# Performance work log

Hardware: AMD Instinct MI355X
Metric: run time of the kernel (lower is better)

Reference implementation:

```python
import jax, jax.numpy as jnp
import numpy as np

B, C, T, V = 64, 64, 128, 25   # batch, in_channels, frames, joints
R = 8                          # rel_channels = in_channels // rel_reduction
TS = 9                         # time_step (temporal taps of dynamic adjacency)
OUT = 64                       # out_channels (conv3)


def setup_inputs() -> dict:
    key = jax.random.key(0)
    ks = jax.random.split(key, 10)
    p = lambda k, shape: jax.random.normal(k, shape, jnp.float32) * 0.05
    return {
        'x':  jax.random.normal(ks[0], (B, C, T, V), jnp.float32),
        'A':  jax.random.normal(ks[1], (V, V), jnp.float32) * 0.1,
        'W1': p(ks[2], (R, C)),       'b1': p(ks[3], (R,)),
        'W2': p(ks[4], (R, C)),       'b2': p(ks[5], (R,)),
        'W4': p(ks[6], (C * TS, R)),  'b4': p(ks[7], (C * TS,)),
        'W3': p(ks[8], (OUT, C)),     'b3': p(ks[9], (OUT,)),
    }


def reference(x, A, W1, b1, W2, b2, W4, b4, W3, b3):
    alpha = 1.0
    # conv1/conv2: 1x1 Conv2d then mean over time (dim -2). 1x1 conv is linear,
    # so mean(conv(x)) == einsum/T + bias.  -> (B, R, V)
    x1 = jnp.einsum('rc,bctv->brv', W1, x) / T + b1[None, :, None]
    x2 = jnp.einsum('rc,bctv->brv', W2, x) / T + b2[None, :, None]
    # tanh relation: (B, R, V, 1) - (B, R, 1, V) -> (B, R, V, V)
    rel = jnp.tanh(x1[:, :, :, None] - x2[:, :, None, :])
    # conv4 (1x1): rel_channels -> C*TS dynamic adjacency, + static A
    Adyn = jnp.einsum('or,brij->boij', W4, rel) + b4[None, :, None, None]
    Adyn = Adyn * alpha + A[None, None]                      # (B, C*TS, V, V)
    # reshape(B, C, TS, V, V).permute(0,1,3,4,2): per-(b,c) temporal graph kernel
    Wk = Adyn.reshape(B, C, TS, V, V).transpose(0, 1, 3, 4, 2)  # (B, C, V, V, TS)
    # x -> (B, C, V, T), causal left-pad by TS-1 (matches F.pad(x, (TS-1, 0)))
    xp = jnp.pad(x.transpose(0, 1, 3, 2), ((0, 0), (0, 0), (0, 0), (TS - 1, 0)))
    # Grouped conv1d loop over V vertices, fused into TS tap-wise einsums:
    # z[b,c,t,i] = sum_{v,k} xp[b,c,v,t+k] * Wk[b,c,v,i,k]   (stride=1)
    z = jnp.zeros((B, C, T, V), x.dtype)
    for k in range(TS):  # small fixed tap loop
        z = z + jnp.einsum('bcvt,bcvi->bcti', xp[..., k:k + T], Wk[..., k])
    # conv3: 1x1 Conv2d C -> OUT
    out = jnp.einsum('oc,bctv->botv', W3, z) + b3[None, :, None, None]
    return out
```

## Files before the change

kernel.cpp:

```cpp
#include <hip/hip_runtime.h>
#include <hip/hip_bf16.h>

#define BB 64
#define CC 64
#define TT_ 128
#define VV 25
#define RR 8
#define TS_ 9
#define OO 64
#define VCH 5

typedef __hip_bfloat16 bf16;
typedef __attribute__((ext_vector_type(8))) short short8;
typedef __attribute__((ext_vector_type(4))) short s16x4;
typedef __attribute__((ext_vector_type(4))) float f32x4;

__device__ __forceinline__ unsigned short f2b(float f) {
    bf16 h = __float2bfloat16(f);
    return __builtin_bit_cast(unsigned short, h);
}

__global__ __launch_bounds__(256) void k_mean(const float* __restrict__ x,
                                              float* __restrict__ xm) {
    __shared__ float smf[800];
    int bc = blockIdx.x;
    int tid = threadIdx.x;
    const float4* p4 = (const float4*)(x + (size_t)bc * TT_ * VV);
    if (tid < 200) {
        float4 a = p4[tid];
        float4 b = p4[tid + 200];
        float4 c = p4[tid + 400];
        float4 d = p4[tid + 600];
        float4 s;
        s.x = a.x + b.x + c.x + d.x;
        s.y = a.y + b.y + c.y + d.y;
        s.z = a.z + b.z + c.z + d.z;
        s.w = a.w + b.w + c.w + d.w;
        ((float4*)smf)[tid] = s;
    }
    __syncthreads();
    if (tid < VV) {
        float tot = 0.f;
        #pragma unroll
        for (int m = 0; m < 32; m++) tot += smf[tid + VV * m];
        xm[bc * VV + tid] = tot * (1.0f / TT_);
    }
}

__global__ __launch_bounds__(256) void k_rel(const float* __restrict__ xm,
                                             const float* __restrict__ W1,
                                             const float* __restrict__ b1,
                                             const float* __restrict__ W2,
                                             const float* __restrict__ b2,
                                             float* __restrict__ rel) {
    __shared__ float xms[CC * VV];
    __shared__ float x1s[RR][VCH];
    __shared__ float x2s[RR][VV];
    int b = blockIdx.x / 5, g = blockIdx.x % 5;
    int v0 = g * VCH;
    int tid = threadIdx.x;
    for (int i = tid; i < CC * VV; i += 256) xms[i] = xm[b * CC * VV + i];
    __syncthreads();
    if (tid < 240) {
        if (tid < 40) {
            int r = tid / VCH, vl = tid % VCH;
            float s1 = b1[r];
            for (int c = 0; c < CC; c++) s1 += W1[r * CC + c] * xms[c * VV + v0 + vl];
            x1s[r][vl] = s1;
        } else {
            int t = tid - 40;
            int r = t / VV, i = t % VV;
            float s2 = b2[r];
            for (int c = 0; c < CC; c++) s2 += W2[r * CC + c] * xms[c * VV + i];
            x2s[r][i] = s2;
        }
    }
    __syncthreads();
    float* relb = rel + (size_t)b * VV * VV * RR + (size_t)v0 * VV * RR;
    for (int idx = tid; idx < VCH * VV * RR; idx += 256) {
        int r = idx % RR;
        int i = (idx / RR) % VV;
        int vl = idx / (RR * VV);
        float d = x1s[r][vl] - x2s[r][i];
        float e = __expf(2.0f * d);
        relb[idx] = (e - 1.0f) / (e + 1.0f);
    }
}

__global__ __launch_bounds__(512, 8) void k_z(const float* __restrict__ x,
                                              const float* __restrict__ Ag,
                                              const float* __restrict__ W4,
                                              const float* __restrict__ b4,
                                              const float* __restrict__ rel,
                                              bf16* __restrict__ zws) {
    __shared__ __align__(16) unsigned short xpadB[136 * 40];
    __shared__ __align__(16) unsigned short AdbS[TS_ * 32 * 40];

    int tid = threadIdx.x;
    int bc = blockIdx.x;
    int b = bc / CC, c = bc % CC;

    if (tid < 128) ((unsigned int*)xpadB)[(tid >> 4) * 20 + (tid & 15)] = 0u;
    if (tid >= 128 && tid < 256) {
        int base = (8 + (tid - 128)) * 40 + 25;
        #pragma unroll
        for (int k = 0; k < 7; k++) xpadB[base + k] = 0;
    }
    if (tid >= 224) {
        int base = (tid - 224) * 40 + 25;
        #pragma unroll
        for (int k = 0; k < 7; k++) AdbS[base + k] = 0;
    }
    const float4* xg4 = (const float4*)(x + (size_t)bc * TT_ * VV);
    for (int i4 = tid; i4 < TT_ * VV / 4; i4 += 512) {
        float4 f = xg4[i4];
        int idx = i4 * 4;
        int t = idx / VV, v = idx - t * VV;
        float fe[4] = {f.x, f.y, f.z, f.w};
        #pragma unroll
        for (int e = 0; e < 4; e++) {
            xpadB[(t + 8) * 40 + v] = f2b(fe[e]);
            v++;
            if (v == VV) { v = 0; t++; }
        }
    }

    const float* relb = rel + (size_t)b * VV * VV * RR;
    const float* W4c = W4 + c * TS_ * RR;
    const float* b4c = b4 + c * TS_;
    for (int task = tid; task < VV * VV; task += 512) {
        int v = task / VV, i = task % VV;
        const float4* r4 = (const float4*)(relb + (size_t)task * RR);
        float4 ra = r4[0], rb_ = r4[1];
        float av = Ag[task];
        #pragma unroll
        for (int s = 0; s < TS_; s++) {
            float a2 = b4c[s] + av;
            a2 += W4c[s*8+0] * ra.x  + W4c[s*8+1] * ra.y
                + W4c[s*8+2] * ra.z  + W4c[s*8+3] * ra.w;
            a2 += W4c[s*8+4] * rb_.x + W4c[s*8+5] * rb_.y
                + W4c[s*8+6] * rb_.z + W4c[s*8+7] * rb_.w;
            AdbS[(s * 32 + i) * 40 + v] = f2b(a2);
        }
    }
    __syncthreads();

    int lane = tid & 63, wv = tid >> 6;
    int ml = lane & 15, qd = lane >> 4;
    f32x4 acc00 = {0.f, 0.f, 0.f, 0.f};
    f32x4 acc01 = acc00;
    int rowA0 = wv * 16 + ml;
    #pragma unroll
    for (int s = 0; s < TS_; s++) {
        short8 a0 = *(const short8*)&xpadB[(rowA0 + s) * 40 + qd * 8];
        short8 b0 = *(const short8*)&AdbS[(s * 32 + ml) * 40 + qd * 8];
        short8 b1 = *(const short8*)&AdbS[(s * 32 + 16 + ml) * 40 + qd * 8];
        acc00 = __builtin_amdgcn_mfma_f32_16x16x32_bf16(a0, b0, acc00, 0, 0, 0);
        acc01 = __builtin_amdgcn_mfma_f32_16x16x32_bf16(a0, b1, acc01, 0, 0, 0);
    }

    bf16* zb = zws + (size_t)bc * TT_ * VV;
    int t0 = wv * 16 + qd * 4;
    int i0 = ml, i1 = 16 + ml;
    #pragma unroll
    for (int r = 0; r < 4; r++)
        zb[(t0 + r) * VV + i0] = __float2bfloat16(acc00[r]);
    if (i1 < VV) {
        #pragma unroll
        for (int r = 0; r < 4; r++)
            zb[(t0 + r) * VV + i1] = __float2bfloat16(acc01[r]);
    }
}

__global__ __launch_bounds__(256) void k_conv3(const bf16* __restrict__ zws,
                                               const float* __restrict__ W3,
                                               const float* __restrict__ b3,
                                               float* __restrict__ out) {
    __shared__ __align__(16) unsigned short w3b[OO * 72];
    __shared__ __align__(16) unsigned short zl[CC * 130];
    __shared__ float b3l[OO];
    int tid = threadIdx.x;
    int b = blockIdx.x / 25, tile = blockIdx.x % 25;
    int tj0 = tile * 128;

    if (tid < OO) b3l[tid] = b3[tid];
    const float4* W3v = (const float4*)W3;
    for (int idx = tid; idx < OO * CC / 4; idx += 256) {
        float4 f = W3v[idx];
        int o = idx >> 4, c4 = (idx & 15) * 4;
        s16x4 s4;
        s4[0] = (short)f2b(f.x);
        s4[1] = (short)f2b(f.y);
        s4[2] = (short)f2b(f.z);
        s4[3] = (short)f2b(f.w);
        *(s16x4*)&w3b[o * 72 + c4] = s4;
    }
    const unsigned int* zg = (const unsigned int*)(zws + (size_t)b * CC * (TT_ * VV));
    for (int idu = tid; idu < CC * 64; idu += 256) {
        int c = idu >> 6, ju = idu & 63;
        ((unsigned int*)zl)[c * 65 + ju] = zg[c * 1600 + (tj0 >> 1) + ju];
    }
    __syncthreads();

    int lane = tid & 63, wv = tid >> 6;
    int ml = lane & 15, qd = lane >> 4;
    f32x4 acc[4][2];
    #pragma unroll
    for (int m = 0; m < 4; m++)
        #pragma unroll
        for (int nl = 0; nl < 2; nl++) acc[m][nl] = (f32x4){0.f, 0.f, 0.f, 0.f};

    #pragma unroll
    for (int k0 = 0; k0 < 2; k0++) {
        short8 a[4];
        #pragma unroll
        for (int m = 0; m < 4; m++)
            a[m] = *(const short8*)&w3b[(m * 16 + ml) * 72 + k0 * 32 + qd * 8];
        #pragma unroll
        for (int nl = 0; nl < 2; nl++) {
            int col = (2 * wv + nl) * 16 + ml;
            int cb = k0 * 32 + qd * 8;
            short8 bf;
            #pragma unroll
            for (int j = 0; j < 8; j++)
                bf[j] = (short)zl[(cb + j) * 130 + col];
            #pragma unroll
            for (int m = 0; m < 4; m++)
                acc[m][nl] = __builtin_amdgcn_mfma_f32_16x16x32_bf16(a[m], bf, acc[m][nl], 0, 0, 0);
        }
    }

    float* ob = out + (size_t)b * OO * (TT_ * VV) + tj0;
    #pragma unroll
    for (int m = 0; m < 4; m++)
        #pragma unroll
        for (int nl = 0; nl < 2; nl++) {
            int col = (2 * wv + nl) * 16 + ml;
            #pragma unroll
            for (int r = 0; r < 4; r++) {
                int o = m * 16 + qd * 4 + r;
                ob[(size_t)o * (TT_ * VV) + col] = acc[m][nl][r] + b3l[o];
            }
        }
}

extern "C" void kernel_launch(void* const* d_in, const int* in_sizes, int n_in,
                              void* d_out, int out_size, void* d_ws, size_t ws_size,
                              hipStream_t stream) {
    const float* x  = (const float*)d_in[0];
    const float* A  = (const float*)d_in[1];
    const float* W1 = (const float*)d_in[2];
    const float* b1 = (const float*)d_in[3];
    const float* W2 = (const float*)d_in[4];
    const float* b2 = (const float*)d_in[5];
    const float* W4 = (const float*)d_in[6];
    const float* b4 = (const float*)d_in[7];
    const float* W3 = (const float*)d_in[8];
    const float* b3 = (const float*)d_in[9];
    float* out = (float*)d_out;

    char* ws = (char*)d_ws;
    float* xm   = (float*)(ws);
    float* rel  = (float*)(ws + 409600);
    bf16*  zws  = (bf16*)(ws + 1689600);

    k_mean <<<BB * CC, 256, 0, stream>>>(x, xm);
    k_rel  <<<BB * 5,  256, 0, stream>>>(xm, W1, b1, W2, b2, rel);
    k_z    <<<BB * CC, 512, 0, stream>>>(x, A, W4, b4, rel, zws);
    k_conv3<<<BB * 25, 256, 0, stream>>>(zws, W3, b3, out);
}
```

Measured before the change: 162.9 us.

## Pre-pack padded bf16 x in k_mean and DMA it into LDS in k_z

k_mean, which already reads x, now also converts it to bf16 in the padded LDS layout that k_z needs and writes that image to a workspace buffer. k_z then loads the ready-made tile straight into LDS with global_load_lds instead of re-reading fp32 x and converting element by element. This halves the bytes k_z reads for x and removes its scattered conversion stores. In exchange k_mean writes an extra bf16 copy of x, k_z's occupancy hint of 8 is dropped, and correctness relies on the global-to-LDS loads completing before the existing barrier.

```diff
diff --git a/kernel.cpp b/kernel.cpp
--- a/kernel.cpp
+++ b/kernel.cpp
@@ -9,6 +9,7 @@
 #define TS_ 9
 #define OO 64
 #define VCH 5
+#define XBF_STRIDE 5632
 
 typedef __hip_bfloat16 bf16;
 typedef __attribute__((ext_vector_type(8))) short short8;
@@ -20,23 +21,45 @@
     return __builtin_bit_cast(unsigned short, h);
 }
 
+__device__ __forceinline__ void putf4(unsigned short* xp, int i4, float4 f) {
+    int idx = i4 * 4;
+    int t = idx / VV, v = idx - t * VV;
+    float fe[4] = {f.x, f.y, f.z, f.w};
+    #pragma unroll
+    for (int e = 0; e < 4; e++) {
+        xp[(t + 8) * 40 + v] = f2b(fe[e]);
+        if (++v == VV) { v = 0; t++; }
+    }
+}
+
 __global__ __launch_bounds__(256) void k_mean(const float* __restrict__ x,
-                                              float* __restrict__ xm) {
+                                              float* __restrict__ xm,
+                                              unsigned short* __restrict__ xbf) {
     __shared__ float smf[800];
+    __shared__ __align__(16) unsigned short xp[141 * 40];
     int bc = blockIdx.x;
     int tid = threadIdx.x;
     const float4* p4 = (const float4*)(x + (size_t)bc * TT_ * VV);
+    float4 a, b, c, d;
     if (tid < 200) {
-        float4 a = p4[tid];
-        float4 b = p4[tid + 200];
-        float4 c = p4[tid + 400];
-        float4 d = p4[tid + 600];
+        a = p4[tid];
+        b = p4[tid + 200];
+        c = p4[tid + 400];
+        d = p4[tid + 600];
+    }
+    for (int i = tid; i < 2820; i += 256) ((unsigned int*)xp)[i] = 0u;
+    __syncthreads();
+    if (tid < 200) {
         float4 s;
         s.x = a.x + b.x + c.x + d.x;
         s.y = a.y + b.y + c.y + d.y;
         s.z = a.z + b.z + c.z + d.z;
         s.w = a.w + b.w + c.w + d.w;
         ((float4*)smf)[tid] = s;
+        putf4(xp, tid,       a);
+        putf4(xp, tid + 200, b);
+        putf4(xp, tid + 400, c);
+        putf4(xp, tid + 600, d);
     }
     __syncthreads();
     if (tid < VV) {
@@ -45,6 +68,9 @@
         for (int m = 0; m < 32; m++) tot += smf[tid + VV * m];
         xm[bc * VV + tid] = tot * (1.0f / TT_);
     }
+    uint4* dst = (uint4*)(xbf + (size_t)bc * XBF_STRIDE);
+    const uint4* src = (const uint4*)xp;
+    for (int i = tid; i < 704; i += 256) dst[i] = src[i];
 }
 
 __global__ __launch_bounds__(256) void k_rel(const float* __restrict__ xm,
@@ -87,42 +113,35 @@
     }
 }
 
-__global__ __launch_bounds__(512, 8) void k_z(const float* __restrict__ x,
-                                              const float* __restrict__ Ag,
-                                              const float* __restrict__ W4,
-                                              const float* __restrict__ b4,
-                                              const float* __restrict__ rel,
-                                              bf16* __restrict__ zws) {
-    __shared__ __align__(16) unsigned short xpadB[136 * 40];
+__global__ __launch_bounds__(512) void k_z(const unsigned short* __restrict__ xbf,
+                                           const float* __restrict__ Ag,
+                                           const float* __restrict__ W4,
+                                           const float* __restrict__ b4,
+                                           const float* __restrict__ rel,
+                                           bf16* __restrict__ zws) {
+    __shared__ __align__(16) unsigned short xpadB[141 * 40];
     __shared__ __align__(16) unsigned short AdbS[TS_ * 32 * 40];
 
     int tid = threadIdx.x;
     int bc = blockIdx.x;
     int b = bc / CC, c = bc % CC;
-
-    if (tid < 128) ((unsigned int*)xpadB)[(tid >> 4) * 20 + (tid & 15)] = 0u;
-    if (tid >= 128 && tid < 256) {
-        int base = (8 + (tid - 128)) * 40 + 25;
-        #pragma unroll
-        for (int k = 0; k < 7; k++) xpadB[base + k] = 0;
+    int lane = tid & 63, w = tid >> 6;
+
+    {
+        const char* gx = (const char*)(xbf + (size_t)bc * XBF_STRIDE);
+        char* lx = (char*)xpadB;
+        __builtin_amdgcn_global_load_lds(
+            (const __attribute__((address_space(1))) void*)(gx + w * 1024 + lane * 16),
+            (__attribute__((address_space(3))) void*)(lx + w * 1024), 16, 0, 0);
+        if (w < 3)
+            __builtin_amdgcn_global_load_lds(
+                (const __attribute__((address_space(1))) void*)(gx + (8 + w) * 1024 + lane * 16),
+                (__attribute__((address_space(3))) void*)(lx + (8 + w) * 1024), 16, 0, 0);
     }
     if (tid >= 224) {
         int base = (tid - 224) * 40 + 25;
         #pragma unroll
         for (int k = 0; k < 7; k++) AdbS[base + k] = 0;
-    }
-    const float4* xg4 = (const float4*)(x + (size_t)bc * TT_ * VV);
-    for (int i4 = tid; i4 < TT_ * VV / 4; i4 += 512) {
-        float4 f = xg4[i4];
-        int idx = i4 * 4;
-        int t = idx / VV, v = idx - t * VV;
-        float fe[4] = {f.x, f.y, f.z, f.w};
-        #pragma unroll
-        for (int e = 0; e < 4; e++) {
-            xpadB[(t + 8) * 40 + v] = f2b(fe[e]);
-            v++;
-            if (v == VV) { v = 0; t++; }
-        }
     }
 
     const float* relb = rel + (size_t)b * VV * VV * RR;
@@ -145,11 +164,10 @@
     }
     __syncthreads();
 
-    int lane = tid & 63, wv = tid >> 6;
     int ml = lane & 15, qd = lane >> 4;
     f32x4 acc00 = {0.f, 0.f, 0.f, 0.f};
     f32x4 acc01 = acc00;
-    int rowA0 = wv * 16 + ml;
+    int rowA0 = w * 16 + ml;
     #pragma unroll
     for (int s = 0; s < TS_; s++) {
         short8 a0 = *(const short8*)&xpadB[(rowA0 + s) * 40 + qd * 8];
@@ -160,7 +178,7 @@
     }
 
     bf16* zb = zws + (size_t)bc * TT_ * VV;
-    int t0 = wv * 16 + qd * 4;
+    int t0 = w * 16 + qd * 4;
     int i0 = ml, i1 = 16 + ml;
     #pragma unroll
     for (int r = 0; r < 4; r++)
@@ -260,12 +278,13 @@
     float* out = (float*)d_out;
 
     char* ws = (char*)d_ws;
-    float* xm   = (float*)(ws);
-    float* rel  = (float*)(ws + 409600);
-    bf16*  zws  = (bf16*)(ws + 1689600);
-
-    k_mean <<<BB * CC, 256, 0, stream>>>(x, xm);
+    float* xm = (float*)(ws);
+    float* rel = (float*)(ws + 409600);
+    bf16*  zws = (bf16*)(ws + 1689600);
+    unsigned short* xbf = (unsigned short*)(ws + 27904000);
+
+    k_mean <<<BB * CC, 256, 0, stream>>>(x, xm, xbf);
     k_rel  <<<BB * 5,  256, 0, stream>>>(xm, W1, b1, W2, b2, rel);
-    k_z    <<<BB * CC, 512, 0, stream>>>(x, A, W4, b4, rel, zws);
+    k_z    <<<BB * CC, 512, 0, stream>>>(xbf, A, W4, b4, rel, zws);
     k_conv3<<<BB * 25, 256, 0, stream>>>(zws, W3, b3, out);
 }
```

After: 165.5 us. Within noise of the previous version (+1.6%).
